# Performance work log

Hardware: AMD Instinct MI355X
Metric: run time of the kernel (lower is better)

## Reference

```python
import jax, jax.numpy as jnp
import numpy as np

N, M, K, R, D = 2048, 64, 2, 512, 1024   # seq len, chunk size, neighbours, neighbour len, model dim
H, L = 16, 1024                           # heads, layer_size
LCH = N // M                              # number of chunks l = 32
DH = L // H
SCALE = 1.0 / (D ** 0.5)                  # source scales by input dim, not head dim


def setup_inputs() -> dict:
    key = jax.random.key(0)
    ks = jax.random.split(key, 6)
    s = 0.02
    return {
        "x": jax.random.normal(ks[0], (N, D), jnp.float32),
        "neighbours": jax.random.normal(ks[1], (LCH, K, R, D), jnp.float32),
        "Wq": jax.random.normal(ks[2], (L, D), jnp.float32) * s,
        "Wk": jax.random.normal(ks[3], (L, D), jnp.float32) * s,
        "Wv": jax.random.normal(ks[4], (L, D), jnp.float32) * s,
        "Wo": jax.random.normal(ks[5], (D, L), jnp.float32) * s,
    }


def _attend(q_in, ctx, Wq, Wk, Wv, Wo):
    # q_in: (B, Q, D) queries; ctx: (B, K, R, D) retrieved neighbours.
    # Batches the per-chunk, per-neighbour Attention calls of the source in one pass,
    # then means over the K neighbour axis (reduce 'k m d -> m d', 'mean').
    B, Q = q_in.shape[0], q_in.shape[1]
    q = (q_in @ Wq.T).reshape(B, Q, H, DH)                     # (B,Q,H,DH)
    kk = (ctx @ Wk.T).reshape(B, K, R, H, DH)                  # (B,K,R,H,DH)
    vv = (ctx @ Wv.T).reshape(B, K, R, H, DH)
    scores = jnp.einsum('bqhe,bkrhe->bkhrq', q, kk) * SCALE    # (B,K,H,R,Q)
    # FAITHFUL quirk: source softmaxes over the QUERY axis (last dim of 'b k q')
    w = jax.nn.softmax(scores, axis=-1)
    o = jnp.einsum('bkhrq,bkrhe->bkqhe', w, vv).reshape(B, K, Q, L)
    z = jnp.einsum('bkql,dl->bkqd', o, Wo)                     # output projection (dropout=0)
    return z.mean(axis=1)                                      # mean over neighbours -> (B,Q,D)


def reference(x, neighbours, Wq, Wk, Wv, Wo):
    # attending_chunks: shift input left by m-1, zero-pad bottom, chunk into (l, m, d)
    att = jnp.concatenate([x[M - 1:], jnp.zeros((M - 1, D), x.dtype)], axis=0).reshape(LCH, M, D)
    # main loop over chunks u in [0, l-2] and their k neighbours, fully batched
    main = _attend(att[:LCH - 1], neighbours[:LCH - 1], Wq, Wk, Wv, Wo)   # (l-1, M, D)
    # last token attends to neighbours[-1]
    last = _attend(x[-1][None, None, :], neighbours[-1][None], Wq, Wk, Wv, Wo)  # (1,1,D)
    body = jnp.concatenate([main.reshape(-1, D), att[-1]], axis=0)        # (N, D)
    # pad top with m-1 zeros, keep first n rows
    out = jnp.concatenate([jnp.zeros((M - 1, D), x.dtype), body[:N - M + 1]], axis=0)
    out = out.at[:M - 1].set(x[:M - 1])
    out = out.at[-1].set(last[0, 0])
    return out
```

## Files before the change

### kernel.cpp

```cpp
#include <hip/hip_runtime.h>
#include <hip/hip_bf16.h>


using u16 = unsigned short;
using u32 = unsigned int;

typedef float  f32x4   __attribute__((ext_vector_type(4)));
typedef __bf16 bf16x8v __attribute__((ext_vector_type(8)));
typedef __bf16 bf16x4v __attribute__((ext_vector_type(4)));
typedef short  s16x4   __attribute__((ext_vector_type(4)));
typedef u16    u16x8   __attribute__((ext_vector_type(8)));
typedef u16    u16x4v  __attribute__((ext_vector_type(4)));

#define SCALE_LOG2E (1.4426950408889634f / 32.0f)

__device__ __forceinline__ u16 f2b(float f){ return __builtin_bit_cast(u16, (__bf16)f); }
__device__ __forceinline__ int swz(int row, int cb){ return row*128 + (cb ^ ((row & 7) << 4)); }

__device__ __forceinline__ void gl_lds16(const void* g, void* l) {
    __builtin_amdgcn_global_load_lds(
        (const __attribute__((address_space(1))) unsigned int*)(unsigned long long)g,
        (__attribute__((address_space(3))) unsigned int*)(unsigned int)(unsigned long long)l,
        16, 0, 0);
}

template<int OM>
__global__ __launch_bounds__(512, 2)
void gemm256(const u16* __restrict__ Ap, int lda,
             const u16* __restrict__ Bp, int ldb,
             void* __restrict__ Cp, void* __restrict__ Cp2,
             int M, int Kc, int nNt)
{
    __shared__ char Ls[131072];
    char* const Abase = Ls;
    char* const Bbase = Ls + 65536;

    const int tid  = threadIdx.x;
    const int lane = tid & 63, wave = tid >> 6;
    const int li = lane & 15, lg = lane >> 4;
    const int wr = wave >> 2, wc = wave & 3;

    const int nwg  = gridDim.x;
    const int lin  = blockIdx.x;
    const int lin2 = (lin & 7) * (nwg >> 3) + (lin >> 3);
    const long bm = (long)(lin2 / nNt) * 256;
    const long bn = (long)(lin2 % nNt) * 256;

    const int srow = tid >> 3;
    const int scol = ((tid & 7) ^ (srow & 7)) << 3;

    const u16* const pA0 = Ap + (bm + srow)*(long)lda + scol;
    const u16* const pA1 = Ap + (bm + 128 + srow)*(long)lda + scol;
    const u16* const pB0 = Bp + (bn + srow)*(long)ldb + scol;
    const u16* const pB1 = Bp + (bn + 128 + srow)*(long)ldb + scol;
    const long l64a = 64*(long)lda, l64b = 64*(long)ldb;

    auto stA = [&](int t, int hh) {
        char* d = Abase + (t & 1)*32768 + hh*16384 + wave*1024;
        const u16* p = (hh ? pA1 : pA0) + (long)t*64;
        gl_lds16(p, d);
        gl_lds16(p + l64a, d + 8192);
    };
    auto stB = [&](int t, int hh) {
        char* d = Bbase + (t & 1)*32768 + hh*16384 + wave*1024;
        const u16* p = (hh ? pB1 : pB0) + (long)t*64;
        gl_lds16(p, d);
        gl_lds16(p + l64b, d + 8192);
    };

    const int NT = Kc >> 6;

    stB(0, 0); stB(0, 1); stA(0, 0); stA(0, 1); stB(1, 0);
    asm volatile("s_waitcnt vmcnt(2)" ::: "memory");
    asm volatile("s_barrier" ::: "memory");

    const int swx = (li & 7) << 4;
    const int cb0 = (lg*16) ^ swx;
    const int cb1 = (64 + lg*16) ^ swx;
    const int brb = (wc & 1)*64 + li;

    f32x4 acc[8][4] = {};
    bf16x8v av[4], aw[4], bv[4];

#define MFMA16(MH, AA, BB)                                                      \
    __builtin_amdgcn_s_setprio(1);                                              \
    _Pragma("unroll") for (int mt = 0; mt < 4; mt++)                            \
        _Pragma("unroll") for (int nt = 0; nt < 4; nt++)                        \
            acc[(MH)*4 + mt][nt] = __builtin_amdgcn_mfma_f32_16x16x32_bf16(     \
                (AA)[mt], (BB)[nt], acc[(MH)*4 + mt][nt], 0, 0, 0);             \
    __builtin_amdgcn_s_setprio(0);
#define RDA(DST, OFS, CB)                                                       \
    _Pragma("unroll") for (int i = 0; i < 4; i++)                               \
        (DST)[i] = *(const bf16x8v*)(At + (li + (OFS) + i*16)*128 + (CB));
#define RDB(DST, CB)                                                            \
    _Pragma("unroll") for (int i = 0; i < 4; i++)                               \
        (DST)[i] = *(const bf16x8v*)(Bt + (brb + i*16)*128 + (CB));

    for (int t = 0; t < NT; ++t) {
        char* At = Abase + (t & 1)*32768 + wr*16384;
        char* Bt = Bbase + (t & 1)*32768 + (wc >> 1)*16384;
        const bool s1 = (t + 1 < NT), s2 = (t + 2 < NT);

        RDA(av, 0, cb0); RDB(bv, cb0);
        if (s1) { stB(t + 1, 1); stA(t + 1, 0); }
        RDA(aw, 64, cb0);
        __builtin_amdgcn_sched_barrier(0);
        MFMA16(0, av, bv);
        if (s1) stA(t + 1, 1);
        RDA(av, 0, cb1);
        __builtin_amdgcn_sched_barrier(0);
        MFMA16(1, aw, bv);
        RDB(bv, cb1); RDA(aw, 64, cb1);
        __builtin_amdgcn_sched_barrier(0);
        MFMA16(0, av, bv);
        asm volatile("s_barrier" ::: "memory");
        if (s2) stB(t + 2, 0);
        MFMA16(1, aw, bv);
        if      (s2) { asm volatile("s_waitcnt vmcnt(2)" ::: "memory"); }
        else if (s1) { asm volatile("s_waitcnt vmcnt(0)" ::: "memory"); }
        asm volatile("s_barrier" ::: "memory");
    }
#undef MFMA16
#undef RDA
#undef RDB

    if (OM == 3 && bn >= 1024) {
        u16* Vt = (u16*)Cp2;
        #pragma unroll
        for (int ai = 0; ai < 8; ai++) {
            const int m0 = wr*128 + (ai >> 2)*64 + (ai & 3)*16 + lg*4;
            #pragma unroll
            for (int nt = 0; nt < 4; nt++) {
                const int n = wc*64 + nt*16 + li;
                f32x4 c = acc[ai][nt];
                bf16x4v w;
                #pragma unroll
                for (int j = 0; j < 4; j++) w[j] = (__bf16)c[j];
                *(bf16x4v*)(Ls + n*512 + ((m0*2) ^ ((n & 31) << 4))) = w;
            }
        }
        __syncthreads();
        const int n    = tid >> 1;
        const int half = (tid & 1) * 128;
        u16* dst = Vt + (bn - 1024 + n)*32768L + bm + half;
        #pragma unroll
        for (int i = 0; i < 16; i++) {
            const int mb = (half + i*8) * 2;
            uint4 v = *(const uint4*)(Ls + n*512 + (mb ^ ((n & 31) << 4)));
            *(uint4*)(dst + i*8) = v;
        }
    } else if (OM == 3) {
        u16* Ka = (u16*)Cp;
        #pragma unroll
        for (int ai = 0; ai < 8; ai++) {
            #pragma unroll
            for (int nt = 0; nt < 4; nt++) {
                f32x4 c = acc[ai][nt];
                const long row0 = bm + wr*128 + (ai >> 2)*64 + (ai & 3)*16 + lg*4;
                const long col  = bn + wc*64 + nt*16 + li;
                #pragma unroll
                for (int j = 0; j < 4; j++)
                    Ka[(row0 + j)*1024 + col] = f2b(c[j]);
            }
        }
    }
}

template<bool AF32, int OM>
__global__ __launch_bounds__(256)
void gemm128(const void* __restrict__ Ap, int lda,
             const u16* __restrict__ Bp, int ldb,
             void* __restrict__ Cp, void* __restrict__ Cp2,
             int M, int Kc, int row_off, int nNt)
{
    __shared__ char As[128*128];
    __shared__ char Bs[128*128];
    const int tid  = threadIdx.x;
    const int lane = tid & 63, wave = tid >> 6;
    const int li = lane & 15, lg = lane >> 4;
    const int wr = wave >> 1, wc = wave & 1;

    const int nwg  = gridDim.x;
    const int lin  = blockIdx.x;
    const int lin2 = (lin & 7) * (nwg >> 3) + (lin >> 3);
    const long bm = (long)(lin2 / nNt) * 128;
    const long bn = (long)(lin2 % nNt) * 128;

    const int grow = wave*32 + (lane >> 3);
    const int gcol = ((lane & 7) ^ (lane >> 3)) << 3;
    const int sr = tid >> 1, sc = (tid & 1) * 32;
    long arow_f = bm + sr; if (arow_f >= M) arow_f = M - 1;
    long arow_g[4];
    #pragma unroll
    for (int j = 0; j < 4; j++) {
        long r = bm + grow + j*8;
        arow_g[j] = (r < M) ? r : (M - 1);
    }

    f32x4 acc[4][4] = {};

    for (int k0 = 0; k0 < Kc; k0 += 64) {
        float4 a4[8];
        if (AF32) {
            const float4* ap = (const float4*)((const float*)Ap + arow_f*lda + k0 + sc);
            #pragma unroll
            for (int i = 0; i < 8; i++) a4[i] = ap[i];
        }
        __syncthreads();
        if (!AF32) {
            #pragma unroll
            for (int j = 0; j < 4; j++)
                gl_lds16((const u16*)Ap + arow_g[j]*(long)lda + k0 + gcol,
                         As + (wave*4 + j)*1024);
        }
        #pragma unroll
        for (int j = 0; j < 4; j++)
            gl_lds16(Bp + (bn + grow + j*8)*(long)ldb + k0 + gcol,
                     Bs + (wave*4 + j)*1024);
        if (AF32) {
            #pragma unroll
            for (int i = 0; i < 4; i++) {
                float4 f0 = a4[2*i], f1 = a4[2*i+1];
                bf16x8v w;
                w[0]=(__bf16)f0.x; w[1]=(__bf16)f0.y; w[2]=(__bf16)f0.z; w[3]=(__bf16)f0.w;
                w[4]=(__bf16)f1.x; w[5]=(__bf16)f1.y; w[6]=(__bf16)f1.z; w[7]=(__bf16)f1.w;
                *(bf16x8v*)(As + swz(sr, sc*2 + i*16)) = w;
            }
        }
        __syncthreads();
        #pragma unroll
        for (int es = 0; es < 2; es++) {
            bf16x8v af[4], bfv[4];
            #pragma unroll
            for (int mt = 0; mt < 4; mt++)
                af[mt] = *(const bf16x8v*)(As + swz(wr*64 + mt*16 + li, es*64 + lg*16));
            #pragma unroll
            for (int nt = 0; nt < 4; nt++)
                bfv[nt] = *(const bf16x8v*)(Bs + swz(wc*64 + nt*16 + li, es*64 + lg*16));
            #pragma unroll
            for (int mt = 0; mt < 4; mt++)
                #pragma unroll
                for (int nt = 0; nt < 4; nt++)
                    acc[mt][nt] = __builtin_amdgcn_mfma_f32_16x16x32_bf16(
                        af[mt], bfv[nt], acc[mt][nt], 0, 0, 0);
        }
    }

    #pragma unroll
    for (int mt = 0; mt < 4; mt++) {
        #pragma unroll
        for (int nt = 0; nt < 4; nt++) {
            f32x4 c = acc[mt][nt];
            const long row0 = bm + wr*64 + mt*16 + lg*4;
            const long col  = bn + wc*64 + nt*16 + li;
            if (OM == 0) {
                u16* C = (u16*)Cp;
                #pragma unroll
                for (int j = 0; j < 4; j++) {
                    long rg = row0 + j;
                    if (rg < M) C[rg*1024 + col] = f2b(c[j]);
                }
            } else if (OM == 2) {
                float* C = (float*)Cp;
                #pragma unroll
                for (int j = 0; j < 4; j++) {
                    long rg = row0 + j;
                    if (rg < M) C[(row_off + rg)*1024 + col] = c[j];
                }
            } else {
                if (col < 1024) {
                    u16* Ka = (u16*)Cp;
                    #pragma unroll
                    for (int j = 0; j < 4; j++) Ka[(row0 + j)*1024 + col] = f2b(c[j]);
                } else {
                    u16* Vt = (u16*)Cp2;
                    bf16x4v w;
                    #pragma unroll
                    for (int j = 0; j < 4; j++) w[j] = (__bf16)c[j];
                    *(bf16x4v*)(Vt + (col - 1024)*32768L + row0) = w;
                }
            }
        }
    }
}

__global__ __launch_bounds__(256)
void attn_kernel(const u16* __restrict__ Qa, const u16* __restrict__ Ka,
                 const u16* __restrict__ Vt, u16* __restrict__ Om)
{
    const int u = blockIdx.x, h = blockIdx.y;
    const int tid = threadIdx.x;
    const int lane = tid & 63, wave = tid >> 6;
    const int li = lane & 15, lg = lane >> 4;

    bf16x8v qf[4][2];
    #pragma unroll
    for (int qt = 0; qt < 4; qt++)
        #pragma unroll
        for (int es = 0; es < 2; es++)
            qf[qt][es] = *(const bf16x8v*)(Qa + (long)(63 + u*64 + qt*16 + li)*1024
                                              + h*64 + es*32 + lg*8);

    f32x4 acc[4][4] = {};

    for (int it = wave; it < 64; it += 4) {
        const int k = it >> 5, rsub = it & 31;
        const long kr = (long)u*1024 + k*512 + rsub*16;

        bf16x8v a0 = *(const bf16x8v*)(Ka + (kr + li)*1024 + h*64 + lg*8);
        bf16x8v a1 = *(const bf16x8v*)(Ka + (kr + li)*1024 + h*64 + 32 + lg*8);
        s16x4 va[4];
        #pragma unroll
        for (int et = 0; et < 4; et++)
            va[et] = *(const s16x4*)(Vt + (long)(h*64 + et*16 + li)*32768 + kr + lg*4);

        f32x4 s[4];
        #pragma unroll
        for (int qt = 0; qt < 4; qt++) {
            f32x4 c = {};
            c = __builtin_amdgcn_mfma_f32_16x16x32_bf16(a0, qf[qt][0], c, 0, 0, 0);
            c = __builtin_amdgcn_mfma_f32_16x16x32_bf16(a1, qf[qt][1], c, 0, 0, 0);
            s[qt] = c;
        }
        float p[4][4];
        #pragma unroll
        for (int qt = 0; qt < 4; qt++)
            #pragma unroll
            for (int j = 0; j < 4; j++)
                p[qt][j] = __builtin_amdgcn_exp2f(s[qt][j]);
        float rz[4];
        #pragma unroll
        for (int j = 0; j < 4; j++) {
            float z = p[0][j] + p[1][j] + p[2][j] + p[3][j];
            z += __shfl_xor(z, 1); z += __shfl_xor(z, 2);
            z += __shfl_xor(z, 4); z += __shfl_xor(z, 8);
            rz[j] = __builtin_amdgcn_rcpf(z);
        }
        s16x4 wf[4];
        #pragma unroll
        for (int qt = 0; qt < 4; qt++) {
            bf16x4v w;
            #pragma unroll
            for (int j = 0; j < 4; j++) w[j] = (__bf16)(p[qt][j] * rz[j]);
            wf[qt] = __builtin_bit_cast(s16x4, w);
        }
        #pragma unroll
        for (int et = 0; et < 4; et++)
            #pragma unroll
            for (int qt = 0; qt < 4; qt++)
                acc[et][qt] = __builtin_amdgcn_mfma_f32_16x16x16bf16_1k(
                    va[et], wf[qt], acc[et][qt], 0, 0, 0);
    }

    __shared__ float Osum[64*64];
    for (int w = 0; w < 4; w++) {
        if (wave == w) {
            #pragma unroll
            for (int et = 0; et < 4; et++)
                #pragma unroll
                for (int qt = 0; qt < 4; qt++)
                    #pragma unroll
                    for (int j = 0; j < 4; j++) {
                        int e = et*16 + lg*4 + j, q = qt*16 + li;
                        if (w == 0) Osum[e*64 + q]  = acc[et][qt][j];
                        else        Osum[e*64 + q] += acc[et][qt][j];
                    }
        }
        __syncthreads();
    }
    const int q = tid & 63, e0 = (tid >> 6) * 16;
    u16x8 o0, o1;
    #pragma unroll
    for (int i = 0; i < 8; i++) {
        o0[i] = f2b(0.5f * Osum[(e0 + i    )*64 + q]);
        o1[i] = f2b(0.5f * Osum[(e0 + 8 + i)*64 + q]);
    }
    u16* dst = Om + (long)(u*64 + q)*1024 + h*64 + e0;
    *(u16x8*)dst       = o0;
    *(u16x8*)(dst + 8) = o1;
}

__global__ __launch_bounds__(256)
void convert_all(const float* __restrict__ Wq, const float* __restrict__ Wk,
                 const float* __restrict__ Wv, const float* __restrict__ Wo,
                 const float* __restrict__ nb, const float* __restrict__ x,
                 u16* __restrict__ wW, u16* __restrict__ Anb,
                 u16* __restrict__ xb, int doA)
{
    const int NW = 524288, NN = 4194304, NX = 262144;
    const int tot = doA ? (NW + NN + NX) : NW;
    const int stride = gridDim.x*256;
    for (int i = blockIdx.x*256 + threadIdx.x; i < tot; i += stride) {
        const float* s; u16* d; float sc = 1.0f;
        if (i < NW) {
            int w = i >> 17;
            long off = (long)(i & 131071) * 8;
            s = (w == 0) ? Wq : (w == 1) ? Wk : (w == 2) ? Wv : Wo;
            s += off;
            d = wW + (long)w*1048576 + off;
            if (w == 0) sc = SCALE_LOG2E;
        } else if (i < NW + NN) {
            long off = (long)(i - NW) * 8;
            s = nb + off; d = Anb + off;
        } else {
            long off = (long)(i - NW - NN) * 8;
            s = x + off; d = xb + off;
        }
        float4 f0 = ((const float4*)s)[0], f1 = ((const float4*)s)[1];
        u16x8 o = { f2b(f0.x*sc), f2b(f0.y*sc), f2b(f0.z*sc), f2b(f0.w*sc),
                    f2b(f1.x*sc), f2b(f1.y*sc), f2b(f1.z*sc), f2b(f1.w*sc) };
        *(u16x8*)d = o;
    }
}

__global__ __launch_bounds__(256)
void last_kernel(const u16* __restrict__ Vt, u16* __restrict__ Om)
{
    const int row  = blockIdx.x*4 + (threadIdx.x >> 6);
    const int lane = threadIdx.x & 63;
    const u16* p = Vt + (long)row*32768 + 31*1024 + lane*16;
    float s = 0.f;
    #pragma unroll
    for (int hf = 0; hf < 2; hf++) {
        bf16x8v v = *(const bf16x8v*)(p + hf*8);
        #pragma unroll
        for (int i = 0; i < 8; i++) s += (float)v[i];
    }
    #pragma unroll
    for (int m = 1; m < 64; m <<= 1) s += __shfl_xor(s, m);
    if (lane == 0) Om[(long)1984*1024 + row] = f2b(0.5f * s);
}

__global__ __launch_bounds__(256)
void copy_head(const float* __restrict__ x, float* __restrict__ out)
{
    int i = blockIdx.x*256 + threadIdx.x;
    ((float4*)out)[i] = ((const float4*)x)[i];
}

extern "C" void kernel_launch(void* const* d_in, const int* in_sizes, int n_in,
                              void* d_out, int out_size, void* d_ws, size_t ws_size,
                              hipStream_t stream)
{
    const float* x  = (const float*)d_in[0];
    const float* nb = (const float*)d_in[1];
    const float* Wq = (const float*)d_in[2];
    const float* Wk = (const float*)d_in[3];
    const float* Wv = (const float*)d_in[4];
    const float* Wo = (const float*)d_in[5];
    float* out = (float*)d_out;
    char*  ws  = (char*)d_ws;

    if (ws_size < (size_t)144*1024*1024) return;
    const bool big = ws_size >= (size_t)212*1024*1024;
    u16* wW  = (u16*)ws;
    u16* Qa  = (u16*)(ws + (size_t) 8*1024*1024);
    u16* Om  = (u16*)(ws + (size_t)12*1024*1024);
    u16* Ka  = (u16*)(ws + (size_t)16*1024*1024);
    u16* Vt  = (u16*)(ws + (size_t)80*1024*1024);
    u16* Anb = (u16*)(ws + (size_t)144*1024*1024);
    u16* xb  = (u16*)(ws + (size_t)208*1024*1024);
    u16* wWq = wW, *wWk = wW + 1048576, *wWo = wW + 3*1048576;

    convert_all<<<dim3(4096), dim3(256), 0, stream>>>(
        Wq, Wk, Wv, Wo, nb, x, wW, Anb, xb, big ? 1 : 0);

    if (big) {
        gemm128<false, 0><<<dim3(128), dim3(256), 0, stream>>>(
            xb, 1024, wWq, 1024, Qa, nullptr, 2048, 1024, 0, 8);
        gemm256<3><<<dim3(1024), dim3(512), 0, stream>>>(
            Anb, 1024, wWk, 1024, Ka, Vt, 32768, 1024, 8);
    } else {
        gemm128<true, 0><<<dim3(128), dim3(256), 0, stream>>>(
            x, 1024, wWq, 1024, Qa, nullptr, 2048, 1024, 0, 8);
        gemm128<true, 3><<<dim3(4096), dim3(256), 0, stream>>>(
            nb, 1024, wWk, 1024, Ka, Vt, 32768, 1024, 0, 16);
    }

    attn_kernel<<<dim3(31, 16), dim3(256), 0, stream>>>(Qa, Ka, Vt, Om);
    last_kernel<<<dim3(256),    dim3(256), 0, stream>>>(Vt, Om);

    gemm128<false, 2><<<dim3(128), dim3(256), 0, stream>>>(
        Om, 1024, wWo, 1024, out, nullptr, 1985, 1024, 63, 8);
    copy_head<<<dim3(63), dim3(256), 0, stream>>>(x, out);
}
```

Measured before the change: 257.0 us.

## Split attention across neighbours into partial kernel plus combine pass

Adds a grid dimension over the two neighbours so each block handles one neighbour's 512 keys, writing fp32 partial outputs into workspace reused from the converted-neighbour buffer. A separate combine kernel averages the two partials and converts them to bf16. The aim is twice as many blocks (992 instead of 496) to fill the GPU better during attention. The cost is an extra fp32 round trip through memory and one more kernel launch. This path only runs when the workspace is large.

```diff
diff --git a/kernel.cpp b/kernel.cpp
--- a/kernel.cpp
+++ b/kernel.cpp
@@ -285,6 +285,113 @@
 }
 
 __global__ __launch_bounds__(256)
+void attn_part(const u16* __restrict__ Qa, const u16* __restrict__ Ka,
+               const u16* __restrict__ Vt, float* __restrict__ Part)
+{
+    const int u = blockIdx.x, h = blockIdx.y, kk = blockIdx.z;
+    const int tid = threadIdx.x;
+    const int lane = tid & 63, wave = tid >> 6;
+    const int li = lane & 15, lg = lane >> 4;
+
+    bf16x8v qf[4][2];
+    #pragma unroll
+    for (int qt = 0; qt < 4; qt++)
+        #pragma unroll
+        for (int es = 0; es < 2; es++)
+            qf[qt][es] = *(const bf16x8v*)(Qa + (long)(63 + u*64 + qt*16 + li)*1024
+                                              + h*64 + es*32 + lg*8);
+
+    f32x4 acc[4][4] = {};
+
+    for (int it = wave; it < 32; it += 4) {
+        const long kr = (long)u*1024 + (long)kk*512 + it*16;
+
+        bf16x8v a0 = *(const bf16x8v*)(Ka + (kr + li)*1024 + h*64 + lg*8);
+        bf16x8v a1 = *(const bf16x8v*)(Ka + (kr + li)*1024 + h*64 + 32 + lg*8);
+        s16x4 va[4];
+        #pragma unroll
+        for (int et = 0; et < 4; et++)
+            va[et] = *(const s16x4*)(Vt + (long)(h*64 + et*16 + li)*32768 + kr + lg*4);
+
+        f32x4 s[4];
+        #pragma unroll
+        for (int qt = 0; qt < 4; qt++) {
+            f32x4 c = {};
+            c = __builtin_amdgcn_mfma_f32_16x16x32_bf16(a0, qf[qt][0], c, 0, 0, 0);
+            c = __builtin_amdgcn_mfma_f32_16x16x32_bf16(a1, qf[qt][1], c, 0, 0, 0);
+            s[qt] = c;
+        }
+        float p[4][4];
+        #pragma unroll
+        for (int qt = 0; qt < 4; qt++)
+            #pragma unroll
+            for (int j = 0; j < 4; j++)
+                p[qt][j] = __builtin_amdgcn_exp2f(s[qt][j]);
+        float rz[4];
+        #pragma unroll
+        for (int j = 0; j < 4; j++) {
+            float z = p[0][j] + p[1][j] + p[2][j] + p[3][j];
+            z += __shfl_xor(z, 1); z += __shfl_xor(z, 2);
+            z += __shfl_xor(z, 4); z += __shfl_xor(z, 8);
+            rz[j] = __builtin_amdgcn_rcpf(z);
+        }
+        s16x4 wf[4];
+        #pragma unroll
+        for (int qt = 0; qt < 4; qt++) {
+            bf16x4v w;
+            #pragma unroll
+            for (int j = 0; j < 4; j++) w[j] = (__bf16)(p[qt][j] * rz[j]);
+            wf[qt] = __builtin_bit_cast(s16x4, w);
+        }
+        #pragma unroll
+        for (int et = 0; et < 4; et++)
+            #pragma unroll
+            for (int qt = 0; qt < 4; qt++)
+                acc[et][qt] = __builtin_amdgcn_mfma_f32_16x16x16bf16_1k(
+                    va[et], wf[qt], acc[et][qt], 0, 0, 0);
+    }
+
+    __shared__ float Osum[4][64*64];
+    #pragma unroll
+    for (int et = 0; et < 4; et++)
+        #pragma unroll
+        for (int qt = 0; qt < 4; qt++)
+            #pragma unroll
+            for (int j = 0; j < 4; j++) {
+                int e = et*16 + lg*4 + j, q = qt*16 + li;
+                Osum[wave][e*64 + q] = acc[et][qt][j];
+            }
+    __syncthreads();
+    const int q = tid & 63, e0 = (tid >> 6) * 16;
+    float* dst = Part + ((long)kk*1984 + u*64 + q)*1024 + h*64 + e0;
+    #pragma unroll
+    for (int i = 0; i < 16; i += 4) {
+        f32x4 v;
+        #pragma unroll
+        for (int j = 0; j < 4; j++) {
+            int e = e0 + i + j;
+            v[j] = Osum[0][e*64 + q] + Osum[1][e*64 + q]
+                 + Osum[2][e*64 + q] + Osum[3][e*64 + q];
+        }
+        *(f32x4*)(dst + i) = v;
+    }
+}
+
+__global__ __launch_bounds__(256)
+void combine_om(const float* __restrict__ Part, u16* __restrict__ Om)
+{
+    const long off = ((long)blockIdx.x*256 + threadIdx.x) * 8;
+    const float4* p0 = (const float4*)(Part + off);
+    const float4* p1 = (const float4*)(Part + 1984L*1024 + off);
+    float4 a0 = p0[0], a1 = p0[1], b0 = p1[0], b1 = p1[1];
+    u16x8 o = { f2b(0.5f*(a0.x+b0.x)), f2b(0.5f*(a0.y+b0.y)),
+                f2b(0.5f*(a0.z+b0.z)), f2b(0.5f*(a0.w+b0.w)),
+                f2b(0.5f*(a1.x+b1.x)), f2b(0.5f*(a1.y+b1.y)),
+                f2b(0.5f*(a1.z+b1.z)), f2b(0.5f*(a1.w+b1.w)) };
+    *(u16x8*)(Om + off) = o;
+}
+
+__global__ __launch_bounds__(256)
 void attn_kernel(const u16* __restrict__ Qa, const u16* __restrict__ Ka,
                  const u16* __restrict__ Vt, u16* __restrict__ Om)
 {
@@ -460,6 +567,7 @@
     u16* Vt  = (u16*)(ws + (size_t)80*1024*1024);
     u16* Anb = (u16*)(ws + (size_t)144*1024*1024);
     u16* xb  = (u16*)(ws + (size_t)208*1024*1024);
+    float* Part = (float*)(ws + (size_t)144*1024*1024);
     u16* wWq = wW, *wWk = wW + 1048576, *wWo = wW + 3*1048576;
 
     convert_all<<<dim3(4096), dim3(256), 0, stream>>>(
@@ -470,15 +578,17 @@
             xb, 1024, wWq, 1024, Qa, nullptr, 2048, 1024, 0, 8);
         gemm256<3><<<dim3(1024), dim3(512), 0, stream>>>(
             Anb, 1024, wWk, 1024, Ka, Vt, 32768, 1024, 8);
+        attn_part<<<dim3(31, 16, 2), dim3(256), 0, stream>>>(Qa, Ka, Vt, Part);
+        combine_om<<<dim3(992), dim3(256), 0, stream>>>(Part, Om);
     } else {
         gemm128<true, 0><<<dim3(128), dim3(256), 0, stream>>>(
             x, 1024, wWq, 1024, Qa, nullptr, 2048, 1024, 0, 8);
         gemm128<true, 3><<<dim3(4096), dim3(256), 0, stream>>>(
             nb, 1024, wWk, 1024, Ka, Vt, 32768, 1024, 0, 16);
-    }
-
-    attn_kernel<<<dim3(31, 16), dim3(256), 0, stream>>>(Qa, Ka, Vt, Om);
-    last_kernel<<<dim3(256),    dim3(256), 0, stream>>>(Vt, Om);
+        attn_kernel<<<dim3(31, 16), dim3(256), 0, stream>>>(Qa, Ka, Vt, Om);
+    }
+
+    last_kernel<<<dim3(256), dim3(256), 0, stream>>>(Vt, Om);
 
     gemm128<false, 2><<<dim3(128), dim3(256), 0, stream>>>(
         Om, 1024, wWo, 1024, out, nullptr, 1985, 1024, 63, 8);
```

After: 268.5 us. +4.5%, slower.
